# Performance work log

Measured on AMD Instinct MI355X. Metric: run time of the kernel, lower is better.

The kernel has to match this reference:

```python
import jax, jax.numpy as jnp
import numpy as np

B, S, H, D = 4, 2048, 16, 128  # batch, seq_len, heads, head_dim
ADJ_SCALE = 0.1


def setup_inputs() -> dict:
    key = jax.random.key(0)
    k1, k2, k3 = jax.random.split(key, 3)
    x = jax.random.normal(k1, (B, S, H, D), dtype=jnp.float32)
    W = jax.random.normal(k2, (D, D), dtype=jnp.float32) * (1.0 / np.sqrt(D))
    b = jax.random.normal(k3, (D,), dtype=jnp.float32) * 0.02
    return {"x": x, "W": W, "b": b}


def reference(x, W, b):
    Bq, Sq, Hq, Dq = x.shape
    # ---- betweenness over [B*H, S, D] ----
    xc = jnp.transpose(x, (0, 2, 1, 3)).reshape(Bq * Hq, Sq, Dq)
    content = jnp.einsum('nsd,ed->nse', xc, W) + b  # Linear(dim, dim)
    # only the (i,i+1) and (i,i+2) distance bands are consumed by the loop
    d01 = jnp.linalg.norm(content[:, :-1] - content[:, 1:], axis=-1)   # [N, S-1]
    d02 = jnp.linalg.norm(content[:, :-2] - content[:, 2:], axis=-1)   # [N, S-2]
    direct = d02
    path = d01[:, :-1] + d01[:, 1:]
    score = jax.nn.relu(1.0 - (path - direct) / jnp.maximum(direct, 1e-6))  # [N, S-2]
    between = jnp.zeros((Bq * Hq, Sq), x.dtype).at[:, 1:Sq - 1].set(score / (Sq - 2))
    between = jnp.transpose(between.reshape(Bq, Hq, Sq), (0, 2, 1))  # [B, S, H]
    # ---- RoPE freq tables ----
    base = 1.0 / (10000.0 ** (jnp.arange(0, Dq, 2, dtype=jnp.float32) / Dq))
    freqs = jnp.arange(Sq, dtype=jnp.float32)[:, None] * base[None, :]  # [S, D/2]
    fcos, fsin = jnp.cos(freqs), jnp.sin(freqs)
    # ---- betweenness-adjusted interpolated RoPE ----
    pos_adj = (between - 0.5) * ADJ_SCALE                               # [B, S, H]
    adj_pos = jnp.clip(jnp.arange(Sq, dtype=jnp.float32)[None, :, None] + pos_adj,
                       0.0, Sq - 1)
    lo = jnp.floor(adj_pos).astype(jnp.int32)
    hi = jnp.ceil(adj_pos).astype(jnp.int32)
    frac = (adj_pos - lo)[..., None]                                    # [B, S, H, 1]
    cos_i = (1.0 - frac) * fcos[lo] + frac * fcos[hi]                   # [B, S, H, D/2]
    sin_i = (1.0 - frac) * fsin[lo] + frac * fsin[hi]
    xe, xo = x[..., 0::2], x[..., 1::2]
    oe = xe * cos_i - xo * sin_i
    oo = xo * cos_i + xe * sin_i
    return jnp.stack([oe, oo], axis=-1).reshape(x.shape)
```

## Files before the change

### kernel.cpp

```cpp
#include <hip/hip_runtime.h>
#include <hip/hip_bf16.h>
#include <math.h>

#define S_LEN 2048
#define NH    64
#define TS    62
#define NTILE 33

typedef __attribute__((ext_vector_type(8))) short short8;
typedef __attribute__((ext_vector_type(4))) float f32x4;

__device__ __forceinline__ unsigned short f2bf(float f) {
    unsigned int u = __float_as_uint(f);
    return (unsigned short)((u + 0x7FFFu + ((u >> 16) & 1u)) >> 16);
}

__global__ __launch_bounds__(256) void k_misc(const float* __restrict__ W,
                                              unsigned short* __restrict__ Wbf,
                                              float2* __restrict__ tab)
{
    int bid = blockIdx.x;
    if (bid < 512) {
        int tid = bid * 256 + threadIdx.x;
        int j = tid & 63;
        int s = tid >> 6;
        float base = powf(10000.f, -(float)(2 * j) * (1.f / 128.f));
        float fr = (float)s * base;
        tab[tid] = make_float2(cosf(fr), sinf(fr));
    } else {
        int idx = (bid - 512) * 256 + threadIdx.x;
        Wbf[idx] = f2bf(W[idx]);
    }
}

__global__ __launch_bounds__(256) void k_dist(const float* __restrict__ x,
                                              const unsigned short* __restrict__ Wbf,
                                              float* __restrict__ d01,
                                              float* __restrict__ d02)
{
    __shared__ char smem[52224];
    unsigned short* Xs  = (unsigned short*)smem;
    unsigned short* Wsh = (unsigned short*)(smem + 17408);
    float*          Cs  = (float*)smem;

    const int tile = blockIdx.x;
    const int n    = blockIdx.y;
    const int bb   = n >> 4, hh = n & 15;
    const int s0   = tile * TS;
    const int t    = threadIdx.x;
    const int w    = t >> 6;
    const int l    = t & 63;
    const int m    = l & 15;
    const int q    = l >> 4;

    #pragma unroll
    for (int i = 0; i < 8; i++) {
        int idx = t + 256 * i;
        int r   = idx >> 5;
        int c4  = idx & 31;
        float4 v = *(const float4*)&x[(((size_t)(bb * S_LEN + s0 + r) * 16 + hh)) * 128 + c4 * 4];
        ushort4 p;
        p.x = f2bf(v.x); p.y = f2bf(v.y); p.z = f2bf(v.z); p.w = f2bf(v.w);
        *(ushort4*)&Xs[r * 136 + c4 * 4] = p;
    }
    #pragma unroll
    for (int i = 0; i < 8; i++) {
        int idx = t + 256 * i;
        int r   = idx >> 4;
        int c8  = idx & 15;
        uint4 v = *(const uint4*)&Wbf[r * 128 + c8 * 8];
        *(uint4*)&Wsh[r * 136 + c8 * 8] = v;
    }
    __syncthreads();

    f32x4 acc[8];
    #pragma unroll
    for (int ct = 0; ct < 8; ct++) acc[ct] = (f32x4){0.f, 0.f, 0.f, 0.f};

    #pragma unroll
    for (int kk = 0; kk < 4; kk++) {
        short8 a = *(const short8*)&Xs[(16 * w + m) * 136 + kk * 32 + q * 8];
        #pragma unroll
        for (int ct = 0; ct < 8; ct++) {
            short8 b = *(const short8*)&Wsh[(16 * ct + m) * 136 + kk * 32 + q * 8];
            acc[ct] = __builtin_amdgcn_mfma_f32_16x16x32_bf16(a, b, acc[ct], 0, 0, 0);
        }
    }
    __syncthreads();

    #pragma unroll
    for (int ct = 0; ct < 8; ct++) {
        int col   = 16 * ct + m;
        int rbase = 16 * w + q * 4;
        #pragma unroll
        for (int r = 0; r < 4; r++)
            Cs[col * 65 + rbase + r] = acc[ct][r];
    }
    __syncthreads();

    int which = w >> 1;
    int j     = (w & 1) * 32 + (l >> 1);
    int g     = l & 1;
    int lim   = which ? (TS - 1) : TS;
    bool active = (j <= lim);
    float part = 0.f;
    if (active) {
        int r1 = j, r2 = j + 1 + which;
        #pragma unroll 8
        for (int i = 0; i < 64; i++) {
            int e = g + 2 * i;
            float d = Cs[e * 65 + r1] - Cs[e * 65 + r2];
            part += d * d;
        }
    }
    part += __shfl_xor(part, 1);
    if (active && g == 0) {
        float dv = sqrtf(part);
        if (which == 0) d01[n * S_LEN + s0 + j] = dv;
        else            d02[n * S_LEN + s0 + j] = dv;
    }
}

__global__ __launch_bounds__(256) void k_rope4(const float* __restrict__ x,
                                               const float* __restrict__ d01,
                                               const float* __restrict__ d02,
                                               const float2* __restrict__ tab,
                                               float* __restrict__ out)
{
    int tid4 = blockIdx.x * 256 + threadIdx.x;
    int d4   = tid4 & 31;
    int rem  = tid4 >> 5;
    int h    = rem & 15;
    int s    = (rem >> 4) & (S_LEN - 1);
    int b    = rem >> 15;
    int n    = b * 16 + h;

    float bet = 0.f;
    if (s >= 1 && s <= S_LEN - 2) {
        int i = s - 1;
        float p  = d01[n * S_LEN + i] + d01[n * S_LEN + i + 1];
        float dd = d02[n * S_LEN + i];
        float sc = 1.f - (p - dd) / fmaxf(dd, 1e-6f);
        bet = fmaxf(sc, 0.f) * (1.f / (float)(S_LEN - 2));
    }

    float adj = (float)s + (bet - 0.5f) * 0.1f;
    adj = fminf(fmaxf(adj, 0.f), (float)(S_LEN - 1));
    float lof = floorf(adj), hif = ceilf(adj);
    float frac = adj - lof;
    int lo = (int)lof, hi = (int)hif;

    float4 tl = *(const float4*)&tab[lo * 64 + 2 * d4];
    float4 th = *(const float4*)&tab[hi * 64 + 2 * d4];
    float ci0 = (1.f - frac) * tl.x + frac * th.x;
    float si0 = (1.f - frac) * tl.y + frac * th.y;
    float ci1 = (1.f - frac) * tl.z + frac * th.z;
    float si1 = (1.f - frac) * tl.w + frac * th.w;

    float4 xv = ((const float4*)x)[tid4];
    float4 o;
    o.x = xv.x * ci0 - xv.y * si0;
    o.y = xv.y * ci0 + xv.x * si0;
    o.z = xv.z * ci1 - xv.w * si1;
    o.w = xv.w * ci1 + xv.z * si1;
    ((float4*)out)[tid4] = o;
}

extern "C" void kernel_launch(void* const* d_in, const int* in_sizes, int n_in,
                              void* d_out, int out_size, void* d_ws, size_t ws_size,
                              hipStream_t stream)
{
    const float* x = (const float*)d_in[0];
    const float* W = (const float*)d_in[1];
    float* out = (float*)d_out;

    float* ws = (float*)d_ws;
    float* d01 = ws;
    float* d02 = ws + 131072;
    float2* tab = (float2*)(ws + 262144);
    unsigned short* Wbf = (unsigned short*)(ws + 524288);

    k_misc <<<576, 256, 0, stream>>>(W, Wbf, tab);
    k_dist <<<dim3(NTILE, NH), 256, 0, stream>>>(x, Wbf, d01, d02);
    k_rope4<<<16384, 256, 0, stream>>>(x, d01, d02, tab, out);
}
```

Baseline: 137.1 us.

## Fuse W conversion and RoPE table build into the distance kernel

Removes the separate prep kernel. Each distance block now converts W from fp32 to bf16 itself while loading it into shared memory. The cos/sin table is built by 512 extra blocks appended to the distance grid. The block index is remapped so tiles iterate over heads fastest, and the C tile store is padded to a stride of 68 so it can use vector float4 writes. This saves one launch and its gap, in exchange for every block re-reading fp32 W (double the bytes) and a different LDS bank pattern.

Result: no change. 136.2 us (-0.6%).

```diff
diff --git a/kernel.cpp b/kernel.cpp
--- a/kernel.cpp
+++ b/kernel.cpp
@@ -6,6 +6,7 @@
 #define NH    64
 #define TS    62
 #define NTILE 33
+#define NDIST (NTILE * NH)
 
 typedef __attribute__((ext_vector_type(8))) short short8;
 typedef __attribute__((ext_vector_type(4))) float f32x4;
@@ -15,39 +16,34 @@
     return (unsigned short)((u + 0x7FFFu + ((u >> 16) & 1u)) >> 16);
 }
 
-__global__ __launch_bounds__(256) void k_misc(const float* __restrict__ W,
-                                              unsigned short* __restrict__ Wbf,
-                                              float2* __restrict__ tab)
-{
-    int bid = blockIdx.x;
-    if (bid < 512) {
-        int tid = bid * 256 + threadIdx.x;
-        int j = tid & 63;
-        int s = tid >> 6;
-        float base = powf(10000.f, -(float)(2 * j) * (1.f / 128.f));
-        float fr = (float)s * base;
-        tab[tid] = make_float2(cosf(fr), sinf(fr));
-    } else {
-        int idx = (bid - 512) * 256 + threadIdx.x;
-        Wbf[idx] = f2bf(W[idx]);
-    }
-}
-
-__global__ __launch_bounds__(256) void k_dist(const float* __restrict__ x,
-                                              const unsigned short* __restrict__ Wbf,
-                                              float* __restrict__ d01,
-                                              float* __restrict__ d02)
+__global__ __launch_bounds__(256) void k_dm(const float* __restrict__ x,
+                                            const float* __restrict__ W,
+                                            float* __restrict__ d01,
+                                            float* __restrict__ d02,
+                                            float2* __restrict__ tab)
 {
     __shared__ char smem[52224];
     unsigned short* Xs  = (unsigned short*)smem;
     unsigned short* Wsh = (unsigned short*)(smem + 17408);
     float*          Cs  = (float*)smem;
 
-    const int tile = blockIdx.x;
-    const int n    = blockIdx.y;
+    const int bid = blockIdx.x;
+    const int t   = threadIdx.x;
+
+    if (bid >= NDIST) {
+        int tid = (bid - NDIST) * 256 + t;
+        int j = tid & 63;
+        int s = tid >> 6;
+        float base = powf(10000.f, -(float)(2 * j) * (1.f / 128.f));
+        float fr = (float)s * base;
+        tab[tid] = make_float2(cosf(fr), sinf(fr));
+        return;
+    }
+
+    const int tile = bid >> 6;
+    const int n    = bid & 63;
     const int bb   = n >> 4, hh = n & 15;
     const int s0   = tile * TS;
-    const int t    = threadIdx.x;
     const int w    = t >> 6;
     const int l    = t & 63;
     const int m    = l & 15;
@@ -68,8 +64,13 @@
         int idx = t + 256 * i;
         int r   = idx >> 4;
         int c8  = idx & 15;
-        uint4 v = *(const uint4*)&Wbf[r * 128 + c8 * 8];
-        *(uint4*)&Wsh[r * 136 + c8 * 8] = v;
+        float4 a = *(const float4*)&W[r * 128 + c8 * 8];
+        float4 b = *(const float4*)&W[r * 128 + c8 * 8 + 4];
+        ushort4 p0, p1;
+        p0.x = f2bf(a.x); p0.y = f2bf(a.y); p0.z = f2bf(a.z); p0.w = f2bf(a.w);
+        p1.x = f2bf(b.x); p1.y = f2bf(b.y); p1.z = f2bf(b.z); p1.w = f2bf(b.w);
+        *(ushort4*)&Wsh[r * 136 + c8 * 8]     = p0;
+        *(ushort4*)&Wsh[r * 136 + c8 * 8 + 4] = p1;
     }
     __syncthreads();
 
@@ -92,9 +93,7 @@
     for (int ct = 0; ct < 8; ct++) {
         int col   = 16 * ct + m;
         int rbase = 16 * w + q * 4;
-        #pragma unroll
-        for (int r = 0; r < 4; r++)
-            Cs[col * 65 + rbase + r] = acc[ct][r];
+        *(f32x4*)&Cs[col * 68 + rbase] = acc[ct];
     }
     __syncthreads();
 
@@ -109,7 +108,7 @@
         #pragma unroll 8
         for (int i = 0; i < 64; i++) {
             int e = g + 2 * i;
-            float d = Cs[e * 65 + r1] - Cs[e * 65 + r2];
+            float d = Cs[e * 68 + r1] - Cs[e * 68 + r2];
             part += d * d;
         }
     }
@@ -178,9 +177,7 @@
     float* d01 = ws;
     float* d02 = ws + 131072;
     float2* tab = (float2*)(ws + 262144);
-    unsigned short* Wbf = (unsigned short*)(ws + 524288);
 
-    k_misc <<<576, 256, 0, stream>>>(W, Wbf, tab);
-    k_dist <<<dim3(NTILE, NH), 256, 0, stream>>>(x, Wbf, d01, d02);
+    k_dm   <<<NDIST + 512, 256, 0, stream>>>(x, W, d01, d02, tab);
     k_rope4<<<16384, 256, 0, stream>>>(x, d01, d02, tab, out);
 }
```
